# Kernel optimization log

Measured on AMD Instinct MI355X. Metric: run time of the kernel, lower is better.

## Reference

```python
import jax, jax.numpy as jnp
import numpy as np

N_HEAD = 16
N_KV_HEAD = 8
HEAD_DIM = 128
N_EMBED = 2048
EPS = 1.1920929e-07  # torch default eps for fp32 rms_norm


def _apply_rotary_emb(x, cos, sin):
    # x: (B, T, H, D); cos/sin: (1, T, 1, D//2)  (nanochat-style half rotation)
    d = x.shape[-1] // 2
    x1, x2 = x[..., :d], x[..., d:]
    y1 = x1 * cos + x2 * sin
    y2 = -x1 * sin + x2 * cos
    return jnp.concatenate([y1, y2], axis=-1).astype(x.dtype)


def _rms_norm(x):
    return x * jax.lax.rsqrt(jnp.mean(jnp.square(x), axis=-1, keepdims=True) + EPS)


def setup_inputs() -> dict:
    key = jax.random.key(0)
    ks = jax.random.split(key, 5)
    B, T = 2, 2048
    kv_dim = N_KV_HEAD * HEAD_DIM
    x = jax.random.normal(ks[0], (B, T, N_EMBED), dtype=jnp.float32)
    w_attn = jax.random.normal(ks[1], (N_EMBED + 2 * kv_dim, N_EMBED), dtype=jnp.float32) * 0.02
    w_proj = jax.random.normal(ks[2], (N_EMBED, N_EMBED), dtype=jnp.float32) * 0.02
    # realistic RoPE tables
    half = HEAD_DIM // 2
    inv_freq = 1.0 / (10000.0 ** (jnp.arange(half, dtype=jnp.float32) / half))
    freqs = jnp.arange(T, dtype=jnp.float32)[:, None] * inv_freq[None, :]  # (T, half)
    cos = jnp.cos(freqs)[None, :, None, :]
    sin = jnp.sin(freqs)[None, :, None, :]
    return {"x": x, "w_attn": w_attn, "w_proj": w_proj, "cos": cos, "sin": sin}


def reference(x, w_attn, w_proj, cos, sin):
    B, T, C = x.shape
    kv_dim = N_KV_HEAD * HEAD_DIM
    qkv = jnp.einsum('btc,oc->bto', x, w_attn)  # (B, T, C + 2*kv_dim)
    q = qkv[..., :C].reshape(B, T, N_HEAD, HEAD_DIM)
    k = qkv[..., C:C + kv_dim].reshape(B, T, N_KV_HEAD, HEAD_DIM)
    v = qkv[..., C + kv_dim:].reshape(B, T, N_KV_HEAD, HEAD_DIM)
    q = _rms_norm(_apply_rotary_emb(q, cos, sin))
    k = _rms_norm(_apply_rotary_emb(k, cos, sin))
    # GQA: repeat kv heads to match query heads
    rep = N_HEAD // N_KV_HEAD
    k = jnp.repeat(k, rep, axis=2)  # (B, T, n_head, D)
    v = jnp.repeat(v, rep, axis=2)
    scale = 1.0 / jnp.sqrt(jnp.float32(HEAD_DIM))
    scores = jnp.einsum('bqhd,bkhd->bhqk', q, k) * scale  # (B, H, T, T)
    causal = jnp.tril(jnp.ones((T, T), dtype=bool))
    scores = jnp.where(causal[None, None], scores, jnp.finfo(scores.dtype).min)
    attn = jax.nn.softmax(scores, axis=-1)
    y = jnp.einsum('bhqk,bkhd->bqhd', attn, v).reshape(B, T, C)
    return jnp.einsum('btc,oc->bto', y, w_proj)
```

## Files before the change

### kernel.cpp

```cpp
#include <hip/hip_runtime.h>

#define B_ 2
#define T_ 2048
#define NH 16
#define NKV 8
#define HD 128
#define C_ 2048
#define KVD (NKV*HD)
#define QKVD (C_ + 2*KVD)
#define NTOK (B_*T_)

typedef __bf16 bf16_t;
typedef __bf16 bf16x2_t __attribute__((ext_vector_type(2)));
typedef __bf16 bf16x4_t __attribute__((ext_vector_type(4)));
typedef __bf16 bf16x8_t __attribute__((ext_vector_type(8)));
typedef float f32x4_t __attribute__((ext_vector_type(4)));
typedef float f32x16_t __attribute__((ext_vector_type(16)));
typedef int i32x4_t __attribute__((ext_vector_type(4)));

__device__ __forceinline__ f32x4_t mfma16(bf16x8_t a, bf16x8_t b, f32x4_t c) {
  return __builtin_amdgcn_mfma_f32_16x16x32_bf16(a, b, c, 0, 0, 0);
}
__device__ __forceinline__ f32x16_t mfma32(bf16x8_t a, bf16x8_t b, f32x16_t c) {
  return __builtin_amdgcn_mfma_f32_32x32x16_bf16(a, b, c, 0, 0, 0);
}
__device__ __forceinline__ f32x16_t zero16() {
  f32x16_t z;
  #pragma unroll
  for (int i = 0; i < 16; i++) z[i] = 0.f;
  return z;
}
__device__ __forceinline__ int pk2(float a, float b) {
  bf16x2_t t; t[0] = (bf16_t)a; t[1] = (bf16_t)b;
  return __builtin_bit_cast(int, t);
}

#define GLDS16(gp, lp) __builtin_amdgcn_global_load_lds( \
    (const __attribute__((address_space(1))) void*)(gp), \
    (__attribute__((address_space(3))) void*)(lp), 16, 0, 0)

#define CFENCE() asm volatile("" ::: "memory")

__global__ __launch_bounds__(256) void cvt3_kernel(const float* __restrict__ s0, bf16_t* __restrict__ d0,
                                                   const float* __restrict__ s1, bf16_t* __restrict__ d1,
                                                   const float* __restrict__ s2, bf16_t* __restrict__ d2) {
  int bid = blockIdx.x;
  const float* s; bf16_t* d; int off;
  if (bid < 8192)       { s = s0; d = d0; off = bid; }
  else if (bid < 16384) { s = s1; d = d1; off = bid - 8192; }
  else                  { s = s2; d = d2; off = bid - 16384; }
  int i = (off * 256 + threadIdx.x) * 4;
  const float4 v = *(const float4*)(s + i);
  bf16x4_t o;
  o[0] = (bf16_t)v.x; o[1] = (bf16_t)v.y; o[2] = (bf16_t)v.z; o[3] = (bf16_t)v.w;
  *(bf16x4_t*)(d + i) = o;
}

__global__ __launch_bounds__(512, 1) void gemm8p(const bf16_t* __restrict__ A,
                                                 const bf16_t* __restrict__ Bm,
                                                 bf16_t* __restrict__ Cb,
                                                 int M, int N, int K) {
  __shared__ __align__(16) bf16_t As[2][256 * 64];
  __shared__ __align__(16) bf16_t Bs[2][256 * 64];
  int tid = threadIdx.x;
  int wave = tid >> 6, lane = tid & 63;
  int quad = lane >> 4, l16 = lane & 15;
  int wm = wave >> 2, wn = wave & 3;
  int gx = gridDim.x, nwg = gx * gridDim.y;
  int flat = blockIdx.y * gx + blockIdx.x;
  int swz = (flat & 7) * (nwg >> 3) + (flat >> 3);
  int bm = (swz / gx) * 256, bn = (swz % gx) * 256;
  int scol = ((tid & 7) ^ ((tid >> 3) & 7)) * 8;
  int srow = tid >> 3;
  const bf16_t* pa = A + (size_t)(bm + srow) * K + scol;
  const bf16_t* pb = Bm + (size_t)(bn + srow) * K + scol;

#define STAGE_A8(buf, tile, h) { \
    GLDS16(pa + (size_t)((h)*128 + 0) * K + (size_t)(tile)*64, &As[buf][((h)*128 + 0 + wave*8)*64]); \
    GLDS16(pa + (size_t)((h)*128 + 64) * K + (size_t)(tile)*64, &As[buf][((h)*128 + 64 + wave*8)*64]); }
#define STAGE_B8(buf, tile, h) { \
    GLDS16(pb + (size_t)((h)*128 + 0) * K + (size_t)(tile)*64, &Bs[buf][((h)*128 + 0 + wave*8)*64]); \
    GLDS16(pb + (size_t)((h)*128 + 64) * K + (size_t)(tile)*64, &Bs[buf][((h)*128 + 64 + wave*8)*64]); }

  f32x4_t acc[8][4];
  #pragma unroll
  for (int i = 0; i < 8; i++)
    #pragma unroll
    for (int j = 0; j < 4; j++) acc[i][j] = (f32x4_t){0.f, 0.f, 0.f, 0.f};

  int nt = K >> 6;
  STAGE_A8(0, 0, 0); STAGE_A8(0, 0, 1); STAGE_B8(0, 0, 0); STAGE_B8(0, 0, 1);
  STAGE_B8(1, 1, 0); STAGE_B8(1, 1, 1);
  asm volatile("s_waitcnt vmcnt(4)" ::: "memory");
  CFENCE(); __builtin_amdgcn_s_barrier(); CFENCE();

  for (int s = 0; s < nt; ++s) {
    int b = s & 1;
    bf16x8_t bfr[4][2];
    #pragma unroll
    for (int jph = 0; jph < 4; ++jph) {
      if (jph == 0) {
        #pragma unroll
        for (int ni = 0; ni < 4; ni++)
          #pragma unroll
          for (int kh = 0; kh < 2; kh++)
            bfr[ni][kh] = *(const bf16x8_t*)&Bs[b][(wn*64 + ni*16 + l16)*64 + (((kh*4 + quad) ^ (l16 & 7))*8)];
      }
      bf16x8_t af[2][2];
      #pragma unroll
      for (int i = 0; i < 2; i++)
        #pragma unroll
        for (int kh = 0; kh < 2; kh++)
          af[i][kh] = *(const bf16x8_t*)&As[b][(wm*128 + (jph*2 + i)*16 + l16)*64 + (((kh*4 + quad) ^ (l16 & 7))*8)];
      if (jph == 0) { if (s + 1 < nt) STAGE_A8(1 - b, s + 1, 0); }
      if (jph == 1) { if (s + 1 < nt) STAGE_A8(1 - b, s + 1, 1); }
      if (jph == 2) { if (s + 2 < nt) STAGE_B8(b, s + 2, 0); }
      if (jph == 3) {
        if (s + 2 < nt) {
          STAGE_B8(b, s + 2, 1);
          asm volatile("s_waitcnt vmcnt(4)" ::: "memory");
        } else {
          asm volatile("s_waitcnt vmcnt(0)" ::: "memory");
        }
      }
      CFENCE(); __builtin_amdgcn_s_barrier(); CFENCE();
      __builtin_amdgcn_s_setprio(1);
      #pragma unroll
      for (int kh = 0; kh < 2; kh++)
        #pragma unroll
        for (int i = 0; i < 2; i++)
          #pragma unroll
          for (int ni = 0; ni < 4; ni++)
            acc[jph*2 + i][ni] = mfma16(af[i][kh], bfr[ni][kh], acc[jph*2 + i][ni]);
      __builtin_amdgcn_s_setprio(0);
      CFENCE(); __builtin_amdgcn_s_barrier(); CFENCE();
    }
  }
  #pragma unroll
  for (int mi = 0; mi < 8; mi++)
    #pragma unroll
    for (int ni = 0; ni < 4; ni++) {
      int row0 = bm + wm*128 + mi*16 + quad*4;
      int col  = bn + wn*64 + ni*16 + l16;
      #pragma unroll
      for (int r = 0; r < 4; r++)
        Cb[(size_t)(row0 + r) * N + col] = (bf16_t)acc[mi][ni][r];
    }
#undef STAGE_A8
#undef STAGE_B8
}

template<int BM>
__global__ __launch_bounds__(512, 1) void gemm_nt2(const bf16_t* __restrict__ A,
                                                   const bf16_t* __restrict__ Bm,
                                                   float* __restrict__ Cf, bf16_t* __restrict__ Cb,
                                                   int M, int N, int K) {
  constexpr int MR = BM / 32;
  constexpr int RA = BM / 64;
  __shared__ __align__(16) bf16_t As[2][BM * 64];
  __shared__ __align__(16) bf16_t Bs[2][256 * 64];
  int tid = threadIdx.x;
  int wave = tid >> 6, lane = tid & 63;
  int quad = lane >> 4, l16 = lane & 15;
  int wm = wave >> 2, wn = wave & 3;
  int gx = gridDim.x;
  int nwg = gx * gridDim.y;
  int flat = blockIdx.y * gx + blockIdx.x;
  int swz = (flat & 7) * (nwg >> 3) + (flat >> 3);
  int bm = (swz / gx) * BM, bn = (swz % gx) * 256;
  int scol = (((tid & 7) ^ ((tid >> 3) & 7))) * 8;
  const bf16_t* pa = A + (size_t)(bm + (tid >> 3)) * K + scol;
  const bf16_t* pb = Bm + (size_t)(bn + (tid >> 3)) * K + scol;

  f32x4_t acc[MR][4];
  #pragma unroll
  for (int i = 0; i < MR; i++)
    #pragma unroll
    for (int j = 0; j < 4; j++) acc[i][j] = (f32x4_t){0.f, 0.f, 0.f, 0.f};

  int nt = K >> 6;
  #pragma unroll
  for (int r = 0; r < RA; r++) GLDS16(pa + (size_t)(r * 64) * K, &As[0][(r * 64 + wave * 8) * 64]);
  #pragma unroll
  for (int r = 0; r < 4; r++)  GLDS16(pb + (size_t)(r * 64) * K, &Bs[0][(r * 64 + wave * 8) * 64]);
  __syncthreads();

  for (int t = 0; t < nt; t++) {
    int cur = t & 1;
    if (t + 1 < nt) {
      int k1 = (t + 1) * 64;
      #pragma unroll
      for (int r = 0; r < RA; r++) GLDS16(pa + (size_t)(r * 64) * K + k1, &As[1 - cur][(r * 64 + wave * 8) * 64]);
      #pragma unroll
      for (int r = 0; r < 4; r++)  GLDS16(pb + (size_t)(r * 64) * K + k1, &Bs[1 - cur][(r * 64 + wave * 8) * 64]);
    }
    bf16x8_t bfr[4][2];
    #pragma unroll
    for (int ni = 0; ni < 4; ni++)
      #pragma unroll
      for (int kh = 0; kh < 2; kh++) {
        int blk = (kh * 4 + quad) ^ (l16 & 7);
        bfr[ni][kh] = *(const bf16x8_t*)&Bs[cur][(wn * 64 + ni * 16 + l16) * 64 + blk * 8];
      }
    #pragma unroll
    for (int g = 0; g < MR / 2; g++) {
      bf16x8_t af[2][2];
      #pragma unroll
      for (int i = 0; i < 2; i++)
        #pragma unroll
        for (int kh = 0; kh < 2; kh++) {
          int blk = (kh * 4 + quad) ^ (l16 & 7);
          af[i][kh] = *(const bf16x8_t*)&As[cur][(wm * (BM / 2) + (g * 2 + i) * 16 + l16) * 64 + blk * 8];
        }
      #pragma unroll
      for (int kh = 0; kh < 2; kh++)
        #pragma unroll
        for (int i = 0; i < 2; i++)
          #pragma unroll
          for (int ni = 0; ni < 4; ni++)
            acc[g * 2 + i][ni] = mfma16(af[i][kh], bfr[ni][kh], acc[g * 2 + i][ni]);
    }
    __syncthreads();
  }
  #pragma unroll
  for (int mi = 0; mi < MR; mi++)
    #pragma unroll
    for (int ni = 0; ni < 4; ni++) {
      int row0 = bm + wm * (BM / 2) + mi * 16 + quad * 4;
      int col  = bn + wn * 64 + ni * 16 + l16;
      if (Cb) {
        #pragma unroll
        for (int r = 0; r < 4; r++)
          Cb[(size_t)(row0 + r) * N + col] = (bf16_t)acc[mi][ni][r];
      } else {
        #pragma unroll
        for (int r = 0; r < 4; r++)
          Cf[(size_t)(row0 + r) * N + col] = acc[mi][ni][r];
      }
    }
}

__global__ __launch_bounds__(256) void rope_norm_kernel(const bf16_t* __restrict__ qkv,
    const float* __restrict__ cosb, const float* __restrict__ sinb,
    bf16_t* __restrict__ qb, bf16_t* __restrict__ kb) {
  int token = blockIdx.y;
  int slot = blockIdx.x * 4 + (threadIdx.x >> 6);
  int lane = threadIdx.x & 63;
  int b = token >> 11, s = token & 2047;
  const bf16_t* row = qkv + (size_t)token * QKVD;
  int base_in = (slot < 16) ? slot * HD : C_ + (slot - 16) * HD;
  float x1 = (float)row[base_in + lane];
  float x2 = (float)row[base_in + 64 + lane];
  float c = cosb[s*64 + lane], sn = sinb[s*64 + lane];
  float y1 = x1*c + x2*sn;
  float y2 = x2*c - x1*sn;
  float ss = y1*y1 + y2*y2;
  ss += __shfl_xor(ss, 1);  ss += __shfl_xor(ss, 2);  ss += __shfl_xor(ss, 4);
  ss += __shfl_xor(ss, 8);  ss += __shfl_xor(ss, 16); ss += __shfl_xor(ss, 32);
  float r = rsqrtf(ss * (1.0f/128.0f) + 1.1920929e-07f);
  bf16_t* dst;
  if (slot < 16) {
    r *= 0.08838834764831845f * 1.4426950408889634f;
    dst = qb + ((size_t)(b*NH + slot) * T_ + s) * HD;
  } else {
    dst = kb + ((size_t)(b*NKV + (slot-16)) * T_ + s) * HD;
  }
  dst[lane]      = (bf16_t)(y1 * r);
  dst[lane + 64] = (bf16_t)(y2 * r);
}

__global__ __launch_bounds__(256) void transpose_v(const bf16_t* __restrict__ qkv,
                                                   bf16_t* __restrict__ vt) {
  __shared__ bf16_t TT[64*136];
  int bk = blockIdx.y;
  int b = bk >> 3, kv = bk & 7;
  int s0 = blockIdx.x * 64;
  int tid = threadIdx.x;
  int row = tid >> 2, c0 = (tid & 3) * 32;
  const bf16_t* src = qkv + (size_t)(b*T_ + s0 + row) * QKVD + C_ + KVD + kv*HD + c0;
  #pragma unroll
  for (int s4 = 0; s4 < 4; s4++)
    *(bf16x8_t*)&TT[row*136 + c0 + s4*8] = *(const bf16x8_t*)(src + s4*8);
  __syncthreads();
  #pragma unroll
  for (int s2 = 0; s2 < 2; s2++) {
    int d = (tid >> 2) + s2*64;
    #pragma unroll
    for (int s = 0; s < 2; s++) {
      int g = (tid & 3) * 8 + s*32;
      bf16x8_t pk;
      #pragma unroll
      for (int e = 0; e < 8; e++) pk[e] = TT[(g + e)*136 + d];
      *(bf16x8_t*)(vt + ((size_t)bk * HD + d) * T_ + s0 + g) = pk;
    }
  }
}

__global__ __launch_bounds__(512, 1) void attn_kernel(const bf16_t* __restrict__ qb,
    const bf16_t* __restrict__ kb, const bf16_t* __restrict__ vt, bf16_t* __restrict__ yb) {
  __shared__ __align__(16) bf16_t Ks[2][2][64*136];
  __shared__ __align__(16) bf16_t Vs[2][2][128*72];
  int L = blockIdx.x;
  int bh = L & 31;
  int qt = 15 - (L >> 5);
  int b = bh >> 4, h = bh & 15, kvh = h >> 1;
  int tid = threadIdx.x;
  int wv = tid >> 6;
  int g  = wv >> 2;
  int sq = wv & 3;
  int lane = tid & 63;
  int l32 = lane & 31, half = lane >> 5;
  int t256 = tid & 255;
  const bf16_t* Qp = qb + (size_t)bh * T_ * HD;
  const bf16_t* Kp = kb + (size_t)(b*NKV + kvh) * T_ * HD;
  const bf16_t* Vt = vt + (size_t)(b*NKV + kvh) * HD * T_;

  int krow = t256 >> 2, kcb = (t256 & 3) * 32;
  int vd = t256 >> 1,  vcb = (t256 & 1) * 32;

  int h0 = qt + 1;
  int kt0 = g * h0;

  int qrow = qt*128 + sq*32 + l32;
  bf16x8_t qf[8];
  #pragma unroll
  for (int kc = 0; kc < 8; kc++)
    qf[kc] = *(const bf16x8_t*)(Qp + (size_t)qrow * HD + kc*16 + half*8);

  float mrow = -1e30f, lrow = 0.f;
  f32x16_t o[4];
  #pragma unroll
  for (int mb = 0; mb < 4; mb++) o[mb] = zero16();

  bf16x8_t kreg[4], vreg[4];
  {
    const bf16_t* srck = Kp + (size_t)(kt0*64 + krow) * HD + kcb;
    const bf16_t* srcv = Vt + (size_t)vd * T_ + kt0*64 + vcb;
    #pragma unroll
    for (int s2 = 0; s2 < 4; s2++) { kreg[s2] = *(const bf16x8_t*)(srck + s2*8);
                                     vreg[s2] = *(const bf16x8_t*)(srcv + s2*8); }
  }
  #pragma unroll
  for (int s2 = 0; s2 < 4; s2++) { *(bf16x8_t*)&Ks[g][0][krow*136 + kcb + s2*8] = kreg[s2];
                                   *(bf16x8_t*)&Vs[g][0][vd*72   + vcb + s2*8] = vreg[s2]; }

  for (int t = 0; t < h0; t++) {
    __syncthreads();
    int cur = t & 1;
    if (t + 1 < h0) {
      int k1 = (kt0 + t + 1) * 64;
      const bf16_t* srck = Kp + (size_t)(k1 + krow) * HD + kcb;
      const bf16_t* srcv = Vt + (size_t)vd * T_ + k1 + vcb;
      #pragma unroll
      for (int s2 = 0; s2 < 4; s2++) { kreg[s2] = *(const bf16x8_t*)(srck + s2*8);
                                       vreg[s2] = *(const bf16x8_t*)(srcv + s2*8); }
    }
    int k0 = (kt0 + t) * 64;
    f32x16_t sacc[2];
    sacc[0] = zero16(); sacc[1] = zero16();
    #pragma unroll
    for (int kc = 0; kc < 8; kc++)
      #pragma unroll
      for (int mb = 0; mb < 2; mb++) {
        bf16x8_t kf = *(const bf16x8_t*)&Ks[g][cur][(mb*32 + l32)*136 + kc*16 + half*8];
        sacc[mb] = mfma32(kf, qf[kc], sacc[mb]);
      }
    if (k0 + 63 > qt*128 + sq*32) {
      #pragma unroll
      for (int mb = 0; mb < 2; mb++)
        #pragma unroll
        for (int r = 0; r < 16; r++) {
          int key = k0 + mb*32 + (r&3) + 8*(r>>2) + 4*half;
          if (key > qrow) sacc[mb][r] = -1e30f;
        }
    }
    float mx = -1e30f;
    #pragma unroll
    for (int mb = 0; mb < 2; mb++)
      #pragma unroll
      for (int r = 0; r < 16; r++) mx = fmaxf(mx, sacc[mb][r]);
    mx = fmaxf(mx, __shfl_xor(mx, 32));
    float mnew = fmaxf(mrow, mx);
    float alpha = exp2f(mrow - mnew);
    mrow = mnew;
    float rs = 0.f;
    #pragma unroll
    for (int mb = 0; mb < 2; mb++)
      #pragma unroll
      for (int r = 0; r < 16; r++) {
        float p = exp2f(sacc[mb][r] - mnew);
        sacc[mb][r] = p;
        rs += p;
      }
    rs += __shfl_xor(rs, 32);
    lrow = lrow * alpha + rs;
    #pragma unroll
    for (int mb = 0; mb < 4; mb++) o[mb] = o[mb] * alpha;
    int P2[2][4][2];
    #pragma unroll
    for (int mb = 0; mb < 2; mb++)
      #pragma unroll
      for (int gg = 0; gg < 4; gg++) {
        P2[mb][gg][0] = pk2(sacc[mb][4*gg+0], sacc[mb][4*gg+1]);
        P2[mb][gg][1] = pk2(sacc[mb][4*gg+2], sacc[mb][4*gg+3]);
      }
    #pragma unroll
    for (int kc = 0; kc < 4; kc++) {
      int mb = kc >> 1, c = kc & 1;
      int o0 = half ? P2[mb][2*c+1][0] : P2[mb][2*c][0];
      int o1 = half ? P2[mb][2*c+1][1] : P2[mb][2*c][1];
      int s0 = half ? P2[mb][2*c][0]   : P2[mb][2*c+1][0];
      int s1 = half ? P2[mb][2*c][1]   : P2[mb][2*c+1][1];
      int r0 = __shfl_xor(s0, 32);
      int r1 = __shfl_xor(s1, 32);
      i32x4_t wvv;
      wvv[0] = half ? r0 : o0;
      wvv[1] = half ? r1 : o1;
      wvv[2] = half ? o0 : r0;
      wvv[3] = half ? o1 : r1;
      bf16x8_t pf = __builtin_bit_cast(bf16x8_t, wvv);
      #pragma unroll
      for (int mbd = 0; mbd < 4; mbd++) {
        bf16x8_t vf = *(const bf16x8_t*)&Vs[g][cur][(mbd*32 + l32)*72 + kc*16 + half*8];
        o[mbd] = mfma32(vf, pf, o[mbd]);
      }
    }
    if (t + 1 < h0) {
      #pragma unroll
      for (int s2 = 0; s2 < 4; s2++) { *(bf16x8_t*)&Ks[g][1-cur][krow*136 + kcb + s2*8] = kreg[s2];
                                       *(bf16x8_t*)&Vs[g][1-cur][vd*72   + vcb + s2*8] = vreg[s2]; }
    }
  }
  __syncthreads();
  float* MG = (float*)Vs;
  int mbase = (sq*64 + lane) * 66;
  if (g == 1) {
    #pragma unroll
    for (int mb = 0; mb < 4; mb++)
      #pragma unroll
      for (int r = 0; r < 16; r++) MG[mbase + mb*16 + r] = o[mb][r];
    MG[mbase + 64] = mrow;
    MG[mbase + 65] = lrow;
  }
  __syncthreads();
  if (g == 0) {
    float m1 = MG[mbase + 64], l1v = MG[mbase + 65];
    float mm = fmaxf(mrow, m1);
    float a0 = exp2f(mrow - mm), a1 = exp2f(m1 - mm);
    float invl = 1.0f / (lrow * a0 + l1v * a1);
    a0 *= invl; a1 *= invl;
    bf16_t* OL = &((bf16_t*)Ks)[sq * 4352];
    #pragma unroll
    for (int mb = 0; mb < 4; mb++)
      #pragma unroll
      for (int rr = 0; rr < 4; rr++) {
        bf16x4_t pk;
        #pragma unroll
        for (int jj = 0; jj < 4; jj++)
          pk[jj] = (bf16_t)(o[mb][rr*4+jj] * a0 + MG[mbase + mb*16 + rr*4 + jj] * a1);
        *(bf16x4_t*)&OL[l32*136 + mb*32 + rr*8 + half*4] = pk;
      }
    int tok = qt*128 + sq*32 + l32;
    bf16_t* dst = yb + ((size_t)(b*T_ + tok) * NH + h) * HD + half*64;
    #pragma unroll
    for (int jj = 0; jj < 8; jj++)
      *(bf16x8_t*)(dst + jj*8) = *(const bf16x8_t*)&OL[l32*136 + half*64 + jj*8];
  }
}

extern "C" void kernel_launch(void* const* d_in, const int* in_sizes, int n_in,
                              void* d_out, int out_size, void* d_ws, size_t ws_size,
                              hipStream_t stream) {
  const float* x      = (const float*)d_in[0];
  const float* w_attn = (const float*)d_in[1];
  const float* w_proj = (const float*)d_in[2];
  const float* cosb   = (const float*)d_in[3];
  const float* sinb   = (const float*)d_in[4];
  float* out = (float*)d_out;

  bf16_t* xb   = (bf16_t*)d_ws;
  bf16_t* wab  = xb + 8388608;
  bf16_t* wpb  = wab + 8388608;
  bf16_t* qkvb = wpb + 4194304;
  bf16_t* qb   = qkvb + 16777216;
  bf16_t* kb   = qb + 8388608;
  bf16_t* vt   = kb + 4194304;
  bf16_t* yb   = vt + 4194304;

  cvt3_kernel<<<20480, 256, 0, stream>>>(x, xb, w_attn, wab, w_proj, wpb);

  gemm8p<<<dim3(16, 16), 512, 0, stream>>>(xb, wab, qkvb, NTOK, QKVD, C_);

  rope_norm_kernel<<<dim3(6, 4096), 256, 0, stream>>>(qkvb, cosb, sinb, qb, kb);
  transpose_v<<<dim3(32, 16), 256, 0, stream>>>(qkvb, vt);

  attn_kernel<<<512, 512, 0, stream>>>(qb, kb, vt, yb);

  gemm_nt2<128><<<dim3(8, 32), 512, 0, stream>>>(yb, wpb, out, nullptr, NTOK, C_, C_);
}
```

Before: 322.3 us.

## Merge rope and V-transpose kernels, skip lazy rescales, repad attention LDS

Merges the RoPE/norm kernel and the V transpose kernel into one launch, with the block index picking the path, to save a launch and its tail gap. In the attention kernel the LDS row padding for K and V tiles changes from 136/72 to 132/68 to alter the bank mapping. The online softmax now rescales the accumulators only when the row max grows by more than a threshold, and the max and sum reductions become trees. The new padding may cause misaligned 16-byte LDS accesses or bank conflicts, and the lazy rescale relies on exp2 headroom for accuracy.

Measured after the change: 312.1 us. -3.2%, faster.

```diff
diff --git a/kernel.cpp b/kernel.cpp
--- a/kernel.cpp
+++ b/kernel.cpp
@@ -40,6 +40,9 @@
     (__attribute__((address_space(3))) void*)(lp), 16, 0, 0)
 
 #define CFENCE() asm volatile("" ::: "memory")
+
+#define KSTR 132
+#define VSTR 68
 
 __global__ __launch_bounds__(256) void cvt3_kernel(const float* __restrict__ s0, bf16_t* __restrict__ d0,
                                                    const float* __restrict__ s1, bf16_t* __restrict__ d1,
@@ -240,66 +243,67 @@
     }
 }
 
-__global__ __launch_bounds__(256) void rope_norm_kernel(const bf16_t* __restrict__ qkv,
+__global__ __launch_bounds__(256) void rope_tv_kernel(const bf16_t* __restrict__ qkv,
     const float* __restrict__ cosb, const float* __restrict__ sinb,
-    bf16_t* __restrict__ qb, bf16_t* __restrict__ kb) {
-  int token = blockIdx.y;
-  int slot = blockIdx.x * 4 + (threadIdx.x >> 6);
-  int lane = threadIdx.x & 63;
-  int b = token >> 11, s = token & 2047;
-  const bf16_t* row = qkv + (size_t)token * QKVD;
-  int base_in = (slot < 16) ? slot * HD : C_ + (slot - 16) * HD;
-  float x1 = (float)row[base_in + lane];
-  float x2 = (float)row[base_in + 64 + lane];
-  float c = cosb[s*64 + lane], sn = sinb[s*64 + lane];
-  float y1 = x1*c + x2*sn;
-  float y2 = x2*c - x1*sn;
-  float ss = y1*y1 + y2*y2;
-  ss += __shfl_xor(ss, 1);  ss += __shfl_xor(ss, 2);  ss += __shfl_xor(ss, 4);
-  ss += __shfl_xor(ss, 8);  ss += __shfl_xor(ss, 16); ss += __shfl_xor(ss, 32);
-  float r = rsqrtf(ss * (1.0f/128.0f) + 1.1920929e-07f);
-  bf16_t* dst;
-  if (slot < 16) {
-    r *= 0.08838834764831845f * 1.4426950408889634f;
-    dst = qb + ((size_t)(b*NH + slot) * T_ + s) * HD;
+    bf16_t* __restrict__ qb, bf16_t* __restrict__ kb, bf16_t* __restrict__ vt) {
+  __shared__ bf16_t TT[64*136];
+  int bid = blockIdx.x;
+  int tid = threadIdx.x;
+  if (bid < 24576) {
+    int token = bid & 4095;
+    int slot = (bid >> 12) * 4 + (tid >> 6);
+    int lane = tid & 63;
+    int b = token >> 11, s = token & 2047;
+    const bf16_t* row = qkv + (size_t)token * QKVD;
+    int base_in = (slot < 16) ? slot * HD : C_ + (slot - 16) * HD;
+    float x1 = (float)row[base_in + lane];
+    float x2 = (float)row[base_in + 64 + lane];
+    float c = cosb[s*64 + lane], sn = sinb[s*64 + lane];
+    float y1 = x1*c + x2*sn;
+    float y2 = x2*c - x1*sn;
+    float ss = y1*y1 + y2*y2;
+    ss += __shfl_xor(ss, 1);  ss += __shfl_xor(ss, 2);  ss += __shfl_xor(ss, 4);
+    ss += __shfl_xor(ss, 8);  ss += __shfl_xor(ss, 16); ss += __shfl_xor(ss, 32);
+    float r = rsqrtf(ss * (1.0f/128.0f) + 1.1920929e-07f);
+    bf16_t* dst;
+    if (slot < 16) {
+      r *= 0.08838834764831845f * 1.4426950408889634f;
+      dst = qb + ((size_t)(b*NH + slot) * T_ + s) * HD;
+    } else {
+      dst = kb + ((size_t)(b*NKV + (slot-16)) * T_ + s) * HD;
+    }
+    dst[lane]      = (bf16_t)(y1 * r);
+    dst[lane + 64] = (bf16_t)(y2 * r);
   } else {
-    dst = kb + ((size_t)(b*NKV + (slot-16)) * T_ + s) * HD;
-  }
-  dst[lane]      = (bf16_t)(y1 * r);
-  dst[lane + 64] = (bf16_t)(y2 * r);
-}
-
-__global__ __launch_bounds__(256) void transpose_v(const bf16_t* __restrict__ qkv,
-                                                   bf16_t* __restrict__ vt) {
-  __shared__ bf16_t TT[64*136];
-  int bk = blockIdx.y;
-  int b = bk >> 3, kv = bk & 7;
-  int s0 = blockIdx.x * 64;
-  int tid = threadIdx.x;
-  int row = tid >> 2, c0 = (tid & 3) * 32;
-  const bf16_t* src = qkv + (size_t)(b*T_ + s0 + row) * QKVD + C_ + KVD + kv*HD + c0;
-  #pragma unroll
-  for (int s4 = 0; s4 < 4; s4++)
-    *(bf16x8_t*)&TT[row*136 + c0 + s4*8] = *(const bf16x8_t*)(src + s4*8);
-  __syncthreads();
-  #pragma unroll
-  for (int s2 = 0; s2 < 2; s2++) {
-    int d = (tid >> 2) + s2*64;
-    #pragma unroll
-    for (int s = 0; s < 2; s++) {
-      int g = (tid & 3) * 8 + s*32;
-      bf16x8_t pk;
-      #pragma unroll
-      for (int e = 0; e < 8; e++) pk[e] = TT[(g + e)*136 + d];
-      *(bf16x8_t*)(vt + ((size_t)bk * HD + d) * T_ + s0 + g) = pk;
+    int id = bid - 24576;
+    int bk = id & 15;
+    int s0 = (id >> 4) * 64;
+    int b = bk >> 3, kv = bk & 7;
+    int row = tid >> 2, c0 = (tid & 3) * 32;
+    const bf16_t* src = qkv + (size_t)(b*T_ + s0 + row) * QKVD + C_ + KVD + kv*HD + c0;
+    #pragma unroll
+    for (int s4 = 0; s4 < 4; s4++)
+      *(bf16x8_t*)&TT[row*136 + c0 + s4*8] = *(const bf16x8_t*)(src + s4*8);
+    __syncthreads();
+    #pragma unroll
+    for (int s2 = 0; s2 < 2; s2++) {
+      int d = (tid >> 2) + s2*64;
+      #pragma unroll
+      for (int s = 0; s < 2; s++) {
+        int g = (tid & 3) * 8 + s*32;
+        bf16x8_t pk;
+        #pragma unroll
+        for (int e = 0; e < 8; e++) pk[e] = TT[(g + e)*136 + d];
+        *(bf16x8_t*)(vt + ((size_t)bk * HD + d) * T_ + s0 + g) = pk;
+      }
     }
   }
 }
 
 __global__ __launch_bounds__(512, 1) void attn_kernel(const bf16_t* __restrict__ qb,
     const bf16_t* __restrict__ kb, const bf16_t* __restrict__ vt, bf16_t* __restrict__ yb) {
-  __shared__ __align__(16) bf16_t Ks[2][2][64*136];
-  __shared__ __align__(16) bf16_t Vs[2][2][128*72];
+  __shared__ __align__(16) bf16_t Ks[2][2][64*KSTR];
+  __shared__ __align__(16) bf16_t Vs[2][2][128*VSTR];
   int L = blockIdx.x;
   int bh = L & 31;
   int qt = 15 - (L >> 5);
@@ -341,8 +345,8 @@
                                      vreg[s2] = *(const bf16x8_t*)(srcv + s2*8); }
   }
   #pragma unroll
-  for (int s2 = 0; s2 < 4; s2++) { *(bf16x8_t*)&Ks[g][0][krow*136 + kcb + s2*8] = kreg[s2];
-                                   *(bf16x8_t*)&Vs[g][0][vd*72   + vcb + s2*8] = vreg[s2]; }
+  for (int s2 = 0; s2 < 4; s2++) { *(bf16x8_t*)&Ks[g][0][krow*KSTR + kcb + s2*8] = kreg[s2];
+                                   *(bf16x8_t*)&Vs[g][0][vd*VSTR  + vcb + s2*8] = vreg[s2]; }
 
   for (int t = 0; t < h0; t++) {
     __syncthreads();
@@ -362,7 +366,7 @@
     for (int kc = 0; kc < 8; kc++)
       #pragma unroll
       for (int mb = 0; mb < 2; mb++) {
-        bf16x8_t kf = *(const bf16x8_t*)&Ks[g][cur][(mb*32 + l32)*136 + kc*16 + half*8];
+        bf16x8_t kf = *(const bf16x8_t*)&Ks[g][cur][(mb*32 + l32)*KSTR + kc*16 + half*8];
         sacc[mb] = mfma32(kf, qf[kc], sacc[mb]);
       }
     if (k0 + 63 > qt*128 + sq*32) {
@@ -374,28 +378,34 @@
           if (key > qrow) sacc[mb][r] = -1e30f;
         }
     }
-    float mx = -1e30f;
+    float tm[16];
+    #pragma unroll
+    for (int r = 0; r < 16; r++) tm[r] = fmaxf(sacc[0][r], sacc[1][r]);
+    #pragma unroll
+    for (int st = 8; st >= 1; st >>= 1)
+      #pragma unroll
+      for (int r = 0; r < st; r++) tm[r] = fmaxf(tm[r], tm[r + st]);
+    float mx = fmaxf(tm[0], __shfl_xor(tm[0], 32));
+    if (!__all(mx - mrow <= 8.0f)) {
+      float mnew = fmaxf(mrow, mx);
+      float alpha = exp2f(mrow - mnew);
+      mrow = mnew;
+      lrow *= alpha;
+      #pragma unroll
+      for (int mb = 0; mb < 4; mb++) o[mb] = o[mb] * alpha;
+    }
     #pragma unroll
     for (int mb = 0; mb < 2; mb++)
       #pragma unroll
-      for (int r = 0; r < 16; r++) mx = fmaxf(mx, sacc[mb][r]);
-    mx = fmaxf(mx, __shfl_xor(mx, 32));
-    float mnew = fmaxf(mrow, mx);
-    float alpha = exp2f(mrow - mnew);
-    mrow = mnew;
-    float rs = 0.f;
-    #pragma unroll
-    for (int mb = 0; mb < 2; mb++)
-      #pragma unroll
-      for (int r = 0; r < 16; r++) {
-        float p = exp2f(sacc[mb][r] - mnew);
-        sacc[mb][r] = p;
-        rs += p;
-      }
-    rs += __shfl_xor(rs, 32);
-    lrow = lrow * alpha + rs;
-    #pragma unroll
-    for (int mb = 0; mb < 4; mb++) o[mb] = o[mb] * alpha;
+      for (int r = 0; r < 16; r++) sacc[mb][r] = exp2f(sacc[mb][r] - mrow);
+    float ts[16];
+    #pragma unroll
+    for (int r = 0; r < 16; r++) ts[r] = sacc[0][r] + sacc[1][r];
+    #pragma unroll
+    for (int st = 8; st >= 1; st >>= 1)
+      #pragma unroll
+      for (int r = 0; r < st; r++) ts[r] += ts[r + st];
+    lrow += ts[0] + __shfl_xor(ts[0], 32);
     int P2[2][4][2];
     #pragma unroll
     for (int mb = 0; mb < 2; mb++)
@@ -421,14 +431,14 @@
       bf16x8_t pf = __builtin_bit_cast(bf16x8_t, wvv);
       #pragma unroll
       for (int mbd = 0; mbd < 4; mbd++) {
-        bf16x8_t vf = *(const bf16x8_t*)&Vs[g][cur][(mbd*32 + l32)*72 + kc*16 + half*8];
+        bf16x8_t vf = *(const bf16x8_t*)&Vs[g][cur][(mbd*32 + l32)*VSTR + kc*16 + half*8];
         o[mbd] = mfma32(vf, pf, o[mbd]);
       }
     }
     if (t + 1 < h0) {
       #pragma unroll
-      for (int s2 = 0; s2 < 4; s2++) { *(bf16x8_t*)&Ks[g][1-cur][krow*136 + kcb + s2*8] = kreg[s2];
-                                       *(bf16x8_t*)&Vs[g][1-cur][vd*72   + vcb + s2*8] = vreg[s2]; }
+      for (int s2 = 0; s2 < 4; s2++) { *(bf16x8_t*)&Ks[g][1-cur][krow*KSTR + kcb + s2*8] = kreg[s2];
+                                       *(bf16x8_t*)&Vs[g][1-cur][vd*VSTR  + vcb + s2*8] = vreg[s2]; }
     }
   }
   __syncthreads();
@@ -449,7 +459,7 @@
     float a0 = exp2f(mrow - mm), a1 = exp2f(m1 - mm);
     float invl = 1.0f / (lrow * a0 + l1v * a1);
     a0 *= invl; a1 *= invl;
-    bf16_t* OL = &((bf16_t*)Ks)[sq * 4352];
+    bf16_t* OL = &((bf16_t*)Ks)[sq * (32 * KSTR)];
     #pragma unroll
     for (int mb = 0; mb < 4; mb++)
       #pragma unroll
@@ -458,13 +468,13 @@
         #pragma unroll
         for (int jj = 0; jj < 4; jj++)
           pk[jj] = (bf16_t)(o[mb][rr*4+jj] * a0 + MG[mbase + mb*16 + rr*4 + jj] * a1);
-        *(bf16x4_t*)&OL[l32*136 + mb*32 + rr*8 + half*4] = pk;
+        *(bf16x4_t*)&OL[l32*KSTR + mb*32 + rr*8 + half*4] = pk;
       }
     int tok = qt*128 + sq*32 + l32;
     bf16_t* dst = yb + ((size_t)(b*T_ + tok) * NH + h) * HD + half*64;
     #pragma unroll
     for (int jj = 0; jj < 8; jj++)
-      *(bf16x8_t*)(dst + jj*8) = *(const bf16x8_t*)&OL[l32*136 + half*64 + jj*8];
+      *(bf16x8_t*)(dst + jj*8) = *(const bf16x8_t*)&OL[l32*KSTR + half*64 + jj*8];
   }
 }
 
@@ -491,8 +501,7 @@
 
   gemm8p<<<dim3(16, 16), 512, 0, stream>>>(xb, wab, qkvb, NTOK, QKVD, C_);
 
-  rope_norm_kernel<<<dim3(6, 4096), 256, 0, stream>>>(qkvb, cosb, sinb, qb, kb);
-  transpose_v<<<dim3(32, 16), 256, 0, stream>>>(qkvb, vt);
+  rope_tv_kernel<<<25088, 256, 0, stream>>>(qkvb, cosb, sinb, qb, kb, vt);
 
   attn_kernel<<<512, 512, 0, stream>>>(qb, kb, vt, yb);
 
```
